# Optimization experiments

Hardware: AMD Instinct MI355X
Metric: run time of the kernel (lower is better)

Reference implementation:

```python
import jax, jax.numpy as jnp
import numpy as np

N_NODES = 100000
N_EDGES = 1600000
N_GRAPHS = 1024
DIM_IN = 128
DIM_SELF = 16
BN_EPS = 1e-5


def _bn(x, gamma, beta):
    # training-mode BatchNorm1d over dim 0 (biased variance, as torch uses for normalization)
    m = jnp.mean(x, axis=0)
    v = jnp.mean((x - m) ** 2, axis=0)
    return gamma * (x - m) * jax.lax.rsqrt(v + BN_EPS) + beta


def _mlp(x, W1, b1, g, b, W2, b2):
    h = x @ W1 + b1
    h = jax.nn.relu(_bn(h, g, b))
    return h @ W2 + b2


def _gin(h, src, dst, W1, b1, g, b, W2, b2):
    # GINConv with eps=0: (1+eps)*h + sum over in-neighbors, then MLP
    agg = jax.ops.segment_sum(h[src], dst, num_segments=N_NODES)
    return _mlp(h + agg, W1, b1, g, b, W2, b2)


def setup_inputs() -> dict:
    key = jax.random.key(0)
    ks = jax.random.split(key, 16)

    def lin(k, fan_in, fan_out):
        bound = 1.0 / np.sqrt(fan_in)
        k1, k2 = jax.random.split(k)
        W = jax.random.uniform(k1, (fan_in, fan_out), jnp.float32, -bound, bound)
        b = jax.random.uniform(k2, (fan_out,), jnp.float32, -bound, bound)
        return W, b

    inp = {}
    inp['feat'] = jax.random.normal(ks[0], (N_NODES, DIM_IN), jnp.float32)
    inp['self_feat'] = jax.random.normal(ks[1], (N_GRAPHS, DIM_SELF), jnp.float32)
    inp['edge_src'] = jax.random.randint(ks[2], (N_EDGES,), 0, N_NODES, jnp.int32)
    inp['edge_dst'] = jax.random.randint(ks[3], (N_EDGES,), 0, N_NODES, jnp.int32)
    inp['node2graph'] = jnp.sort(jax.random.randint(ks[4], (N_NODES,), 0, N_GRAPHS, jnp.int32))

    inp['g1_W1'], inp['g1_b1'] = lin(ks[5], DIM_IN, 100)
    inp['g1_gamma'] = jnp.ones((100,), jnp.float32)
    inp['g1_beta'] = jnp.zeros((100,), jnp.float32)
    inp['g1_W2'], inp['g1_b2'] = lin(ks[6], 100, 100)

    inp['g2_W1'], inp['g2_b1'] = lin(ks[7], 100, 20)
    inp['g2_gamma'] = jnp.ones((20,), jnp.float32)
    inp['g2_beta'] = jnp.zeros((20,), jnp.float32)
    inp['g2_W2'], inp['g2_b2'] = lin(ks[8], 20, 20)

    inp['fc1_W'], inp['fc1_b'] = lin(ks[9], 20 * DIM_SELF, 32)
    inp['bn1_gamma'] = jnp.ones((32,), jnp.float32)
    inp['bn1_beta'] = jnp.zeros((32,), jnp.float32)
    inp['fc2_W'], inp['fc2_b'] = lin(ks[10], 32, 8)
    inp['bn2_gamma'] = jnp.ones((8,), jnp.float32)
    inp['bn2_beta'] = jnp.zeros((8,), jnp.float32)
    inp['fc3_W'], inp['fc3_b'] = lin(ks[11], 8, 1)
    return inp


def reference(feat, self_feat,
              g1_W1, g1_b1, g1_gamma, g1_beta, g1_W2, g1_b2,
              g2_W1, g2_b1, g2_gamma, g2_beta, g2_W2, g2_b2,
              fc1_W, fc1_b, bn1_gamma, bn1_beta,
              fc2_W, fc2_b, bn2_gamma, bn2_beta,
              fc3_W, fc3_b,
              edge_src, edge_dst, node2graph):
    h = _gin(feat, edge_src, edge_dst, g1_W1, g1_b1, g1_gamma, g1_beta, g1_W2, g1_b2)
    h = jax.nn.relu(h)
    h = _gin(h, edge_src, edge_dst, g2_W1, g2_b1, g2_gamma, g2_beta, g2_W2, g2_b2)
    h = jax.nn.relu(h)  # [N, 20]

    # dgl.mean_nodes: per-graph mean of node features
    sums = jax.ops.segment_sum(h, node2graph, num_segments=N_GRAPHS)  # [B, 20]
    cnts = jax.ops.segment_sum(jnp.ones((N_NODES,), h.dtype), node2graph, num_segments=N_GRAPHS)
    hg = sums / jnp.maximum(cnts, 1.0)[:, None]

    # kronecker fusion: bmm([B,20,1],[B,1,dim_self]) -> flatten
    kron = jnp.einsum('bi,bj->bij', hg, self_feat).reshape(N_GRAPHS, -1)  # [B, 20*dim_self]

    out = jax.nn.relu(_bn(kron @ fc1_W + fc1_b, bn1_gamma, bn1_beta))
    # dropout(0.3) is identity in eval mode
    out = jax.nn.relu(_bn(out @ fc2_W + fc2_b, bn2_gamma, bn2_beta))
    out = out @ fc3_W + fc3_b  # [B, dim_out]
    return out
```

## Files before the change

### kernel.cpp

```cpp
#include <hip/hip_runtime.h>

#define NN 100000
#define NE 1600000
#define NG 1024
#define DIN 128
#define D1 100
#define D2 20
#define DSELF 16
#define BN_EPS 1e-5f

#define NB 391
#define NBLK 782
#define EPB 2048
#define RAWCAP 5120
#define NAGG2 4000
#define NREP 64
#define APITCH 136
#define G1BLK 1563

typedef unsigned int uint;
typedef unsigned short ushort;
typedef __attribute__((ext_vector_type(8))) short bfv8;
typedef __attribute__((ext_vector_type(4))) float fv4;

__device__ inline float bflo(uint x) { return __uint_as_float(x << 16); }
__device__ inline float bfhi(uint x) { return __uint_as_float(x & 0xffff0000u); }
__device__ inline float bfval(ushort h) { return __uint_as_float(((uint)h) << 16); }
__device__ inline uint packbf2(float a, float b) {
    uint ua = __float_as_uint(a), ub = __float_as_uint(b);
    ua += 0x7fffu + ((ua >> 16) & 1u);
    ub += 0x7fffu + ((ub >> 16) & 1u);
    return (ua >> 16) | (ub & 0xffff0000u);
}
__device__ inline ushort bfr(float x) {
    uint u = __float_as_uint(x);
    u += 0x7fffu + ((u >> 16) & 1u);
    return (ushort)(u >> 16);
}

__global__ __launch_bounds__(256) void k_gemm1A1(const float* __restrict__ feat,
                                                 const float* __restrict__ W1,
                                                 ushort* __restrict__ z1bf,
                                                 float* __restrict__ pb1r,
                                                 const int* __restrict__ edst,
                                                 int* __restrict__ pbcount,
                                                 const float* __restrict__ W2,
                                                 const float* __restrict__ W1p,
                                                 ushort* __restrict__ W2fh,
                                                 ushort* __restrict__ W2fl,
                                                 ushort* __restrict__ W1pfh,
                                                 ushort* __restrict__ W1pfl) {
    __shared__ __align__(16) char smem[64 * APITCH * 2 + 112 * APITCH * 2];
    int t = threadIdx.x;
    int blk = blockIdx.x;
    if (blk >= G1BLK) {
        int hb = blk - G1BLK;
        int* h = (int*)smem;
        if (hb < 9) {
#pragma unroll
            for (int i2 = 0; i2 < 8; i2++) {
                int idx = hb * 2048 + i2 * 256 + t;
                int l = (idx >> 3) & 63, j = idx & 7;
                int kq = (l >> 4) * 8 + j;
                int n16 = l & 15;
                if (idx < 14336) {
                    int tile = idx >> 9; int nt = tile >> 2, kk = tile & 3;
                    int k = kk * 32 + kq, n = nt * 16 + n16;
                    float v = (k < 100 && n < 100) ? W2[k * 100 + n] : 0.f;
                    ushort hh = bfr(v);
                    W2fh[idx] = hh; W2fl[idx] = bfr(v - bfval(hh));
                } else {
                    int idx2 = idx - 14336;
                    int tile = idx2 >> 9; int nt = tile >> 2, kk = tile & 3;
                    int k = kk * 32 + kq, n = nt * 16 + n16;
                    float v = (k < 100 && n < 20) ? W1p[k * 20 + n] : 0.f;
                    ushort hh = bfr(v);
                    W1pfh[idx2] = hh; W1pfl[idx2] = bfr(v - bfval(hh));
                }
            }
        }
        for (int i = t; i < NB; i += 256) h[i] = 0;
        __syncthreads();
        int e0 = hb * EPB + t;
#pragma unroll
        for (int i = 0; i < 8; i++) {
            int e = e0 + i * 256;
            if (e < NE) atomicAdd(&h[edst[e] >> 8], 1);
        }
        __syncthreads();
        for (int i = t; i < NB; i += 256) pbcount[i * NBLK + hb] = h[i];
        return;
    }
    ushort* Al = (ushort*)smem;
    ushort* Bt = (ushort*)(smem + 64 * APITCH * 2);
    if (blk == 0) {
        for (int i = t; i < NREP * 200; i += 256) pb1r[i] = 0.f;
    }
    int row0 = blk * 64;
#pragma unroll
    for (int i = 0; i < 8; i++) {
        int p = i * 256 + t;
        int r = p >> 5, cq = p & 31;
        int row = row0 + r; if (row >= NN) row = NN - 1;
        float4 v = *(const float4*)(feat + (size_t)row * DIN + cq * 4);
        ushort* dst = Al + r * APITCH + 4 * cq;
        dst[0] = bfr(v.x); dst[1] = bfr(v.y); dst[2] = bfr(v.z); dst[3] = bfr(v.w);
    }
    for (int p = t; p < 12800; p += 256) {
        int k = p / 100, n = p % 100;
        Bt[n * APITCH + k] = bfr(W1[p]);
    }
    __syncthreads();
    int w = __builtin_amdgcn_readfirstlane(t >> 6);
    int l = t & 63;
    int m16 = l & 15, quad = l >> 4;
    fv4 acc[7];
#pragma unroll
    for (int nt = 0; nt < 7; nt++) acc[nt] = (fv4){0.f, 0.f, 0.f, 0.f};
    const ushort* arow = Al + (w * 16 + m16) * APITCH;
#pragma unroll
    for (int kk = 0; kk < 4; kk++) {
        int kb = kk * 32 + quad * 8;
        bfv8 a = *(const bfv8*)(arow + kb);
#pragma unroll
        for (int nt = 0; nt < 7; nt++) {
            bfv8 b = *(const bfv8*)(Bt + (nt * 16 + m16) * APITCH + kb);
            acc[nt] = __builtin_amdgcn_mfma_f32_16x16x32_bf16(a, b, acc[nt], 0, 0, 0);
        }
    }
    __syncthreads();
    float* Ep = (float*)smem;
#pragma unroll
    for (int nt = 0; nt < 7; nt++) {
        int n = nt * 16 + m16;
        if (n < 100) {
#pragma unroll
            for (int rix = 0; rix < 4; rix++)
                Ep[(w * 16 + quad * 4 + rix) * 101 + n] = acc[nt][rix];
        }
    }
    __syncthreads();
#pragma unroll
    for (int i = 0; i < 13; i++) {
        int p = i * 256 + t;
        if (p < 3200) {
            int rr = p / 50, cc = 2 * (p % 50);
            int row = row0 + rr;
            if (row < NN) {
                float v0 = Ep[rr * 101 + cc], v1 = Ep[rr * 101 + cc + 1];
                *(uint*)(z1bf + (size_t)row * 128 + cc) = packbf2(v0, v1);
            }
        }
    }
}

__global__ __launch_bounds__(1024) void k_csrS1(int* __restrict__ pbcount,
                                                int* __restrict__ btot) {
    __shared__ int s[1024];
    int t = threadIdx.x, b = blockIdx.x;
    int v = (t < NBLK) ? pbcount[b * NBLK + t] : 0;
    s[t] = v;
    __syncthreads();
    for (int off = 1; off < 1024; off <<= 1) {
        int x = (t >= off) ? s[t - off] : 0;
        __syncthreads();
        s[t] += x;
        __syncthreads();
    }
    if (t < NBLK) pbcount[b * NBLK + t] = s[t] - v;
    if (t == 1023) btot[b] = s[t];
}

__global__ __launch_bounds__(256) void k_csrA2(const int* __restrict__ src,
                                               const int* __restrict__ dst,
                                               const int* __restrict__ pbexcl,
                                               const int* __restrict__ btot,
                                               int* __restrict__ ebase_g,
                                               uint* __restrict__ gbuf) {
    __shared__ int gb[NB];
    __shared__ int lo[NB];
    __shared__ int cnt[NB];
    __shared__ int sa[512], sb[512];
    __shared__ uint stage[EPB];
    __shared__ ushort bkts[EPB];
    int t = threadIdx.x, blk = blockIdx.x;
    int o0 = (t < NB) ? btot[t] : 0;
    int o1 = (t + 256 < NB) ? btot[t + 256] : 0;
    sa[t] = o0; sa[t + 256] = o1;
    if (t < NB) cnt[t] = 0;
    if (t + 256 < NB) cnt[t + 256] = 0;
    __syncthreads();
    int* sp = sa; int* dp = sb;
    for (int off = 1; off < 512; off <<= 1) {
        dp[t] = sp[t] + ((t >= off) ? sp[t - off] : 0);
        int i2 = t + 256;
        dp[i2] = sp[i2] + ((i2 >= off) ? sp[i2 - off] : 0);
        __syncthreads();
        int* tmp = sp; sp = dp; dp = tmp;
    }
    if (t < NB)       gb[t]       = (sp[t] - o0) + pbexcl[t * NBLK + blk];
    if (t + 256 < NB) gb[t + 256] = (sp[t + 256] - o1) + pbexcl[(t + 256) * NBLK + blk];
    if (blk == 0) {
        if (t < NB)       ebase_g[t]       = sp[t] - o0;
        if (t + 256 < NB) ebase_g[t + 256] = sp[t + 256] - o1;
        if (t == 0)       ebase_g[NB]      = sp[NB - 1];
    }
    __syncthreads();
    int e0 = blk * EPB + t;
    uint pv[8]; int bk[8];
#pragma unroll
    for (int i = 0; i < 8; i++) {
        int e = e0 + i * 256;
        if (e < NE) {
            int d = dst[e];
            bk[i] = d >> 8;
            pv[i] = (uint)src[e] | ((uint)(d & 255) << 17);
            atomicAdd(&cnt[bk[i]], 1);
        } else bk[i] = -1;
    }
    __syncthreads();
    sa[t] = (t < NB) ? cnt[t] : 0;
    sa[t + 256] = (t + 256 < NB) ? cnt[t + 256] : 0;
    __syncthreads();
    sp = sa; dp = sb;
    for (int off = 1; off < 512; off <<= 1) {
        dp[t] = sp[t] + ((t >= off) ? sp[t - off] : 0);
        int i2 = t + 256;
        dp[i2] = sp[i2] + ((i2 >= off) ? sp[i2 - off] : 0);
        __syncthreads();
        int* tmp = sp; sp = dp; dp = tmp;
    }
    if (t < NB)       lo[t]       = sp[t] - cnt[t];
    if (t + 256 < NB) lo[t + 256] = sp[t + 256] - cnt[t + 256];
    __syncthreads();
    if (t < NB) cnt[t] = 0;
    if (t + 256 < NB) cnt[t + 256] = 0;
    __syncthreads();
#pragma unroll
    for (int i = 0; i < 8; i++) {
        if (bk[i] >= 0) {
            int lpos = lo[bk[i]] + atomicAdd(&cnt[bk[i]], 1);
            stage[lpos] = pv[i];
            bkts[lpos] = (ushort)bk[i];
        }
    }
    __syncthreads();
    int cntb = (blk * EPB + EPB <= NE) ? EPB : (NE - blk * EPB);
    for (int i = t; i < cntb; i += 256) {
        int b = bkts[i];
        gbuf[gb[b] + (i - lo[b])] = stage[i];
    }
}

__global__ __launch_bounds__(256) void k_csrB(const uint* __restrict__ gbuf,
                                              const int* __restrict__ ebase,
                                              int* __restrict__ deg,
                                              int* __restrict__ offs,
                                              int* __restrict__ srcS) {
    __shared__ uint raw[RAWCAP];
    __shared__ int srt[RAWCAP];
    __shared__ int pref[256], cur[256];
    int t = threadIdx.x, b = blockIdx.x;
    int e0 = ebase[b], e1 = ebase[b + 1];
    int cnt = e1 - e0; if (cnt > RAWCAP) cnt = RAWCAP;
    cur[t] = 0;
    for (int i = t; i < cnt; i += 256) raw[i] = gbuf[e0 + i];
    __syncthreads();
    for (int i = t; i < cnt; i += 256) atomicAdd(&cur[raw[i] >> 17], 1);
    __syncthreads();
    int v = cur[t];
    pref[t] = v;
    __syncthreads();
    for (int off = 1; off < 256; off <<= 1) {
        int x = (t >= off) ? pref[t - off] : 0;
        __syncthreads();
        pref[t] += x;
        __syncthreads();
    }
    int excl = pref[t] - v;
    int node = b * 256 + t;
    if (node < NN) { deg[node] = v; offs[node] = e0 + excl; }
    cur[t] = excl;
    __syncthreads();
    for (int i = t; i < cnt; i += 256) {
        uint p = raw[i];
        int lpos = atomicAdd(&cur[p >> 17], 1);
        srt[lpos] = (int)(p & 0x1FFFFu);
    }
    __syncthreads();
    for (int i = t; i < cnt; i += 256) srcS[e0 + i] = srt[i];
}

__global__ __launch_bounds__(256) void k_agg1(const ushort* __restrict__ z1bf,
                                              const int* __restrict__ offs,
                                              const int* __restrict__ deg,
                                              const int* __restrict__ srcS,
                                              ushort* __restrict__ u1b,
                                              float* __restrict__ pb1r) {
    __shared__ float part[4][200];
    int t = threadIdx.x;
    int wv = __builtin_amdgcn_readfirstlane(t >> 6);
    int l = t & 63;
    bool act = l < 50;
    const ushort* zc = z1bf + 2 * l;
    float S0 = 0.f, S1 = 0.f, Q0 = 0.f, Q1 = 0.f;
    int n0 = blockIdx.x * 16 + wv * 4;
#pragma unroll 1
    for (int k = 0; k < 4; k++) {
        int n = n0 + k;
        int d = deg[n], base = offs[n];
        float a0 = 0.f, a1 = 0.f, b0 = 0.f, b1 = 0.f;
        float c0 = 0.f, c1 = 0.f, e0 = 0.f, e1 = 0.f;
        int i = 0;
        for (; i + 8 <= d; i += 8) {
            int s0 = srcS[base + i],     s1 = srcS[base + i + 1];
            int s2 = srcS[base + i + 2], s3 = srcS[base + i + 3];
            int s4 = srcS[base + i + 4], s5 = srcS[base + i + 5];
            int s6 = srcS[base + i + 6], s7 = srcS[base + i + 7];
            if (act) {
                uint x0 = *(const uint*)(zc + (size_t)s0 * 128);
                uint x1 = *(const uint*)(zc + (size_t)s1 * 128);
                uint x2 = *(const uint*)(zc + (size_t)s2 * 128);
                uint x3 = *(const uint*)(zc + (size_t)s3 * 128);
                uint x4 = *(const uint*)(zc + (size_t)s4 * 128);
                uint x5 = *(const uint*)(zc + (size_t)s5 * 128);
                uint x6 = *(const uint*)(zc + (size_t)s6 * 128);
                uint x7 = *(const uint*)(zc + (size_t)s7 * 128);
                a0 += bflo(x0); a1 += bfhi(x0);
                b0 += bflo(x1); b1 += bfhi(x1);
                c0 += bflo(x2); c1 += bfhi(x2);
                e0 += bflo(x3); e1 += bfhi(x3);
                a0 += bflo(x4); a1 += bfhi(x4);
                b0 += bflo(x5); b1 += bfhi(x5);
                c0 += bflo(x6); c1 += bfhi(x6);
                e0 += bflo(x7); e1 += bfhi(x7);
            }
        }
        for (; i + 2 <= d; i += 2) {
            int s0 = srcS[base + i], s1 = srcS[base + i + 1];
            if (act) {
                uint x0 = *(const uint*)(zc + (size_t)s0 * 128);
                uint x1 = *(const uint*)(zc + (size_t)s1 * 128);
                a0 += bflo(x0); a1 += bfhi(x0);
                b0 += bflo(x1); b1 += bfhi(x1);
            }
        }
        if (i < d) {
            int s0 = srcS[base + i];
            if (act) {
                uint x0 = *(const uint*)(zc + (size_t)s0 * 128);
                a0 += bflo(x0); a1 += bfhi(x0);
            }
        }
        if (act) {
            uint xs = *(const uint*)(zc + (size_t)n * 128);
            float r0 = (a0 + b0) + (c0 + e0) + bflo(xs);
            float r1 = (a1 + b1) + (c1 + e1) + bfhi(xs);
            *(uint*)(u1b + (size_t)n * 100 + 2 * l) = packbf2(r0, r1);
            S0 += r0; S1 += r1;
            Q0 = fmaf(r0, r0, Q0); Q1 = fmaf(r1, r1, Q1);
        }
    }
    if (act) {
        part[wv][2 * l] = S0;        part[wv][2 * l + 1] = S1;
        part[wv][100 + 2 * l] = Q0;  part[wv][100 + 2 * l + 1] = Q1;
    }
    __syncthreads();
    if (t < 200) {
        float s = part[0][t] + part[1][t] + part[2][t] + part[3][t];
        atomicAdd(&pb1r[(blockIdx.x & (NREP - 1)) * 200 + t], s);
    }
}

__global__ __launch_bounds__(256) void k_m2(const ushort* __restrict__ u1b,
                                            const float* __restrict__ pb1r,
                                            const float* __restrict__ gamma,
                                            const float* __restrict__ beta,
                                            const ushort* __restrict__ W2fh,
                                            const ushort* __restrict__ W2fl,
                                            const float* __restrict__ b2,
                                            const ushort* __restrict__ W1pfh,
                                            const ushort* __restrict__ W1pfl,
                                            ushort* __restrict__ z2bf,
                                            float* __restrict__ pb2r,
                                            float* __restrict__ hgsum) {
    __shared__ __align__(16) ushort Ah[64 * APITCH];
    __shared__ __align__(16) ushort Alo[64 * APITCH];
    __shared__ float red200[200];
    __shared__ float scW[100], shW[100];
    int t = threadIdx.x;
    if (blockIdx.x == 0) {
        for (int i = t; i < NREP * 40; i += 256) pb2r[i] = 0.f;
        for (int i = t; i < NG * D2; i += 256) hgsum[i] = 0.f;
    }
    if (t < 200) {
        float s = 0.f;
#pragma unroll 8
        for (int r = 0; r < NREP; r++) s += pb1r[r * 200 + t];
        red200[t] = s;
    }
    for (int p = t; p < 896; p += 256) {
        int r = p / 14, c = 100 + 2 * (p % 14);
        *(uint*)(Ah + r * APITCH + c) = 0u;
        *(uint*)(Alo + r * APITCH + c) = 0u;
    }
    __syncthreads();
    if (t < 100) {
        float S = red200[t], Q = red200[100 + t];
        float mean = S * (1.f / NN);
        float var = Q * (1.f / NN) - mean * mean;
        float inv = rsqrtf(var + BN_EPS);
        float s = gamma[t] * inv;
        scW[t] = s;
        shW[t] = beta[t] - mean * s;
    }
    __syncthreads();
    int row0 = blockIdx.x * 64;
#pragma unroll
    for (int i = 0; i < 13; i++) {
        int p = i * 256 + t;
        if (p < 3200) {
            int r = p / 50, c = 2 * (p % 50);
            int row = row0 + r; if (row >= NN) row = NN - 1;
            uint x = *(const uint*)(u1b + (size_t)row * 100 + c);
            float y0 = fmaxf(bflo(x) * scW[c] + shW[c], 0.f);
            float y1 = fmaxf(bfhi(x) * scW[c + 1] + shW[c + 1], 0.f);
            ushort h0 = bfr(y0), h1 = bfr(y1);
            ushort l0 = bfr(y0 - bfval(h0)), l1 = bfr(y1 - bfval(h1));
            *(uint*)(Ah + r * APITCH + c) = (uint)h0 | ((uint)h1 << 16);
            *(uint*)(Alo + r * APITCH + c) = (uint)l0 | ((uint)l1 << 16);
        }
    }
    __syncthreads();
    int w = __builtin_amdgcn_readfirstlane(t >> 6);
    int l = t & 63;
    int m16 = l & 15, quad = l >> 4;
    fv4 acc[7];
#pragma unroll
    for (int nt = 0; nt < 7; nt++) acc[nt] = (fv4){0.f, 0.f, 0.f, 0.f};
    {
        const ushort* arH = Ah + (w * 16 + m16) * APITCH;
        const ushort* arL = Alo + (w * 16 + m16) * APITCH;
#pragma unroll
        for (int kk = 0; kk < 4; kk++) {
            int kb = kk * 32 + quad * 8;
            bfv8 ah = *(const bfv8*)(arH + kb);
            bfv8 al = *(const bfv8*)(arL + kb);
#pragma unroll
            for (int nt = 0; nt < 7; nt++) {
                int fo = ((nt * 4 + kk) << 9) + l * 8;
                bfv8 bh = *(const bfv8*)(W2fh + fo);
                bfv8 bl = *(const bfv8*)(W2fl + fo);
                acc[nt] = __builtin_amdgcn_mfma_f32_16x16x32_bf16(ah, bh, acc[nt], 0, 0, 0);
                acc[nt] = __builtin_amdgcn_mfma_f32_16x16x32_bf16(ah, bl, acc[nt], 0, 0, 0);
                acc[nt] = __builtin_amdgcn_mfma_f32_16x16x32_bf16(al, bh, acc[nt], 0, 0, 0);
            }
        }
    }
    __syncthreads();
#pragma unroll
    for (int nt = 0; nt < 7; nt++) {
        int n = nt * 16 + m16;
        float bb = (n < 100) ? b2[n] : 0.f;
#pragma unroll
        for (int rix = 0; rix < 4; rix++) {
            int r = w * 16 + quad * 4 + rix;
            float hv = (n < 100) ? fmaxf(acc[nt][rix] + bb, 0.f) : 0.f;
            ushort hh = bfr(hv);
            Ah[r * APITCH + n] = hh;
            Alo[r * APITCH + n] = bfr(hv - bfval(hh));
        }
    }
    __syncthreads();
    fv4 acc2[2];
    acc2[0] = (fv4){0.f, 0.f, 0.f, 0.f};
    acc2[1] = (fv4){0.f, 0.f, 0.f, 0.f};
    {
        const ushort* arH = Ah + (w * 16 + m16) * APITCH;
        const ushort* arL = Alo + (w * 16 + m16) * APITCH;
#pragma unroll
        for (int kk = 0; kk < 4; kk++) {
            int kb = kk * 32 + quad * 8;
            bfv8 ah = *(const bfv8*)(arH + kb);
            bfv8 al = *(const bfv8*)(arL + kb);
#pragma unroll
            for (int nt = 0; nt < 2; nt++) {
                int fo = ((nt * 4 + kk) << 9) + l * 8;
                bfv8 bh = *(const bfv8*)(W1pfh + fo);
                bfv8 bl = *(const bfv8*)(W1pfl + fo);
                acc2[nt] = __builtin_amdgcn_mfma_f32_16x16x32_bf16(ah, bh, acc2[nt], 0, 0, 0);
                acc2[nt] = __builtin_amdgcn_mfma_f32_16x16x32_bf16(ah, bl, acc2[nt], 0, 0, 0);
                acc2[nt] = __builtin_amdgcn_mfma_f32_16x16x32_bf16(al, bh, acc2[nt], 0, 0, 0);
            }
        }
    }
#pragma unroll
    for (int nt = 0; nt < 2; nt++) {
        int c = nt * 16 + m16;
        if (c < 20) {
#pragma unroll
            for (int rix = 0; rix < 4; rix++) {
                int row = row0 + w * 16 + quad * 4 + rix;
                if (row < NN) z2bf[(size_t)row * 32 + c] = bfr(acc2[nt][rix]);
            }
        }
    }
}

__global__ __launch_bounds__(256) void k_agg2(const ushort* __restrict__ z2bf,
                                              const int* __restrict__ offs,
                                              const int* __restrict__ deg,
                                              const int* __restrict__ srcS,
                                              float* __restrict__ u2,
                                              float* __restrict__ pb2r) {
    __shared__ float ls[500], lq[500];
    int t = threadIdx.x;
    int n = blockIdx.x * 25 + t / 10;
    int c2 = 2 * (t % 10);
    float r0 = 0.f, r1 = 0.f;
    if (t < 250 && n < NN) {
        int d = deg[n], base = offs[n];
        const ushort* zc = z2bf + c2;
        float a0 = 0.f, a1 = 0.f, b0 = 0.f, b1 = 0.f;
        float c0 = 0.f, c1 = 0.f, e0 = 0.f, e1 = 0.f;
        int i = 0;
        for (; i + 8 <= d; i += 8) {
            int s0 = srcS[base + i],     s1 = srcS[base + i + 1];
            int s2 = srcS[base + i + 2], s3 = srcS[base + i + 3];
            int s4 = srcS[base + i + 4], s5 = srcS[base + i + 5];
            int s6 = srcS[base + i + 6], s7 = srcS[base + i + 7];
            uint x0 = *(const uint*)(zc + (size_t)s0 * 32);
            uint x1 = *(const uint*)(zc + (size_t)s1 * 32);
            uint x2 = *(const uint*)(zc + (size_t)s2 * 32);
            uint x3 = *(const uint*)(zc + (size_t)s3 * 32);
            uint x4 = *(const uint*)(zc + (size_t)s4 * 32);
            uint x5 = *(const uint*)(zc + (size_t)s5 * 32);
            uint x6 = *(const uint*)(zc + (size_t)s6 * 32);
            uint x7 = *(const uint*)(zc + (size_t)s7 * 32);
            a0 += bflo(x0); a1 += bfhi(x0);
            b0 += bflo(x1); b1 += bfhi(x1);
            c0 += bflo(x2); c1 += bfhi(x2);
            e0 += bflo(x3); e1 += bfhi(x3);
            a0 += bflo(x4); a1 += bfhi(x4);
            b0 += bflo(x5); b1 += bfhi(x5);
            c0 += bflo(x6); c1 += bfhi(x6);
            e0 += bflo(x7); e1 += bfhi(x7);
        }
        for (; i + 2 <= d; i += 2) {
            uint x0 = *(const uint*)(zc + (size_t)srcS[base + i] * 32);
            uint x1 = *(const uint*)(zc + (size_t)srcS[base + i + 1] * 32);
            a0 += bflo(x0); a1 += bfhi(x0);
            b0 += bflo(x1); b1 += bfhi(x1);
        }
        if (i < d) {
            uint x0 = *(const uint*)(zc + (size_t)srcS[base + i] * 32);
            a0 += bflo(x0); a1 += bfhi(x0);
        }
        uint xs = *(const uint*)(zc + (size_t)n * 32);
        r0 = (a0 + b0) + (c0 + e0) + bflo(xs);
        r1 = (a1 + b1) + (c1 + e1) + bfhi(xs);
        *(float2*)(u2 + (size_t)n * D2 + c2) = make_float2(r0, r1);
    }
    if (t < 250) {
        int idx = (t / 10) * 20 + c2;
        ls[idx] = r0;     lq[idx] = r0 * r0;
        ls[idx + 1] = r1; lq[idx + 1] = r1 * r1;
    }
    __syncthreads();
    if (t < 20) {
        float S = 0.f, Q = 0.f;
#pragma unroll
        for (int j = 0; j < 25; j++) { S += ls[j * 20 + t]; Q += lq[j * 20 + t]; }
        int rep = (blockIdx.x & (NREP - 1)) * 40;
        atomicAdd(&pb2r[rep + t], S);
        atomicAdd(&pb2r[rep + 20 + t], Q);
    }
}

__global__ __launch_bounds__(256) void k_m3p(const float* __restrict__ u2,
                                             const float* __restrict__ pb2r,
                                             const float* __restrict__ gamma,
                                             const float* __restrict__ beta,
                                             const float* __restrict__ W2p,
                                             const float* __restrict__ b2p,
                                             const int* __restrict__ n2g,
                                             float* __restrict__ hgsum) {
    __shared__ float X[256][21];
    __shared__ int gl[256];
    __shared__ float red40[40], scB[20], shB[20];
    int t = threadIdx.x;
    if (t < 40) {
        float s = 0.f;
#pragma unroll 8
        for (int r = 0; r < NREP; r++) s += pb2r[r * 40 + t];
        red40[t] = s;
    }
    __syncthreads();
    if (t < 20) {
        float S = red40[t], Q = red40[20 + t];
        float mean = S * (1.f / NN);
        float var = Q * (1.f / NN) - mean * mean;
        float inv = rsqrtf(var + BN_EPS);
        float s = gamma[t] * inv;
        scB[t] = s;
        shB[t] = beta[t] - mean * s;
    }
    __syncthreads();
    int row = blockIdx.x * 256 + t;
    bool valid = row < NN;
    gl[t] = valid ? n2g[row] : -1;
    if (valid) {
        float ya[20];
        const float4* up = (const float4*)(u2 + (size_t)row * D2);
#pragma unroll
        for (int i = 0; i < 5; i++) {
            float4 v = up[i];
            ya[4 * i + 0] = fmaxf(v.x * scB[4 * i + 0] + shB[4 * i + 0], 0.f);
            ya[4 * i + 1] = fmaxf(v.y * scB[4 * i + 1] + shB[4 * i + 1], 0.f);
            ya[4 * i + 2] = fmaxf(v.z * scB[4 * i + 2] + shB[4 * i + 2], 0.f);
            ya[4 * i + 3] = fmaxf(v.w * scB[4 * i + 3] + shB[4 * i + 3], 0.f);
        }
#pragma unroll
        for (int j = 0; j < D2; j++) {
            float h = b2p[j];
#pragma unroll
            for (int k = 0; k < D2; k++) h = fmaf(ya[k], W2p[k * D2 + j], h);
            X[t][j] = fmaxf(h, 0.f);
        }
    } else {
#pragma unroll
        for (int j = 0; j < D2; j++) X[t][j] = 0.f;
    }
    __syncthreads();
    if (t < 160) {
        int seg = t / 20, j = t % 20;
        int i0 = seg * 32, i1 = i0 + 32;
        int gprev = -2;
        float acc = 0.f;
        for (int i = i0; i < i1; i++) {
            int gi = gl[i];
            if (gi != gprev) {
                if (gprev >= 0) atomicAdd(&hgsum[gprev * D2 + j], acc);
                gprev = gi; acc = 0.f;
            }
            acc += X[i][j];
        }
        if (gprev >= 0) atomicAdd(&hgsum[gprev * D2 + j], acc);
    }
}

__global__ void k_head1(const float* __restrict__ hgsum, const int* __restrict__ n2g,
                        const float* __restrict__ sf,
                        const float* __restrict__ fc1W, float* __restrict__ a1) {
    int b = blockIdx.x * 8 + threadIdx.x / 32;
    int c = threadIdx.x % 32;
    if (b >= NG) return;
    int lo = 0, hi2 = NN;
    while (lo < hi2) { int mid = (lo + hi2) >> 1; if (n2g[mid] < b) lo = mid + 1; else hi2 = mid; }
    int s0 = lo;
    hi2 = NN;
    while (lo < hi2) { int mid = (lo + hi2) >> 1; if (n2g[mid] < b + 1) lo = mid + 1; else hi2 = mid; }
    float rc = 1.f / fmaxf((float)(lo - s0), 1.f);
    const float* hgb = hgsum + b * D2;
    const float* sfb = sf + b * DSELF;
    float acc = 0.f;
    for (int i = 0; i < D2; i++) {
        float hv = hgb[i] * rc;
#pragma unroll
        for (int j = 0; j < DSELF; j++)
            acc += hv * sfb[j] * fc1W[(i * DSELF + j) * 32 + c];
    }
    a1[b * 32 + c] = acc;
}

__global__ __launch_bounds__(1024) void k_head2(
    const float* __restrict__ a1, const float* __restrict__ g1,
    const float* __restrict__ be1, const float* __restrict__ fc2W,
    const float* __restrict__ g2, const float* __restrict__ be2,
    const float* __restrict__ fc3W, const float* __restrict__ fc3b,
    float* __restrict__ out) {
    int t = threadIdx.x;
    int lane = t & 63, w = t >> 6;
    __shared__ float s1[16][32], s2[16][32];
    __shared__ float sc[32], sh[32], sc2[8], sh2[8];
    float x[32];
    const float4* ap = (const float4*)(a1 + t * 32);
#pragma unroll
    for (int i = 0; i < 8; i++) {
        float4 v = ap[i];
        x[4 * i] = v.x; x[4 * i + 1] = v.y; x[4 * i + 2] = v.z; x[4 * i + 3] = v.w;
    }
#pragma unroll
    for (int c = 0; c < 32; c++) {
        float v = x[c], q = v * v;
        for (int o = 32; o > 0; o >>= 1) {
            v += __shfl_down(v, o, 64);
            q += __shfl_down(q, o, 64);
        }
        if (lane == 0) { s1[w][c] = v; s2[w][c] = q; }
    }
    __syncthreads();
    if (t < 32) {
        float s = 0.f, q = 0.f;
        for (int ww = 0; ww < 16; ww++) { s += s1[ww][t]; q += s2[ww][t]; }
        float mean = s * (1.f / NG);
        float var = q * (1.f / NG) - mean * mean;
        float inv = rsqrtf(var + BN_EPS);
        float scl = g1[t] * inv;
        sc[t] = scl;
        sh[t] = be1[t] - mean * scl;
    }
    __syncthreads();
#pragma unroll
    for (int c = 0; c < 32; c++) x[c] = fmaxf(x[c] * sc[c] + sh[c], 0.f);
    float y[8];
#pragma unroll
    for (int p = 0; p < 8; p++) {
        float a = 0.f;
#pragma unroll
        for (int c = 0; c < 32; c++) a += x[c] * fc2W[c * 8 + p];
        y[p] = a;
    }
    __syncthreads();
#pragma unroll
    for (int p = 0; p < 8; p++) {
        float v = y[p], q = v * v;
        for (int o = 32; o > 0; o >>= 1) {
            v += __shfl_down(v, o, 64);
            q += __shfl_down(q, o, 64);
        }
        if (lane == 0) { s1[w][p] = v; s2[w][p] = q; }
    }
    __syncthreads();
    if (t < 8) {
        float s = 0.f, q = 0.f;
        for (int ww = 0; ww < 16; ww++) { s += s1[ww][t]; q += s2[ww][t]; }
        float mean = s * (1.f / NG);
        float var = q * (1.f / NG) - mean * mean;
        float inv = rsqrtf(var + BN_EPS);
        float scl = g2[t] * inv;
        sc2[t] = scl;
        sh2[t] = be2[t] - mean * scl;
    }
    __syncthreads();
    float o = fc3b[0];
#pragma unroll
    for (int p = 0; p < 8; p++) {
        float yy = fmaxf(y[p] * sc2[p] + sh2[p], 0.f);
        o += yy * fc3W[p];
    }
    out[t] = o;
}

extern "C" void kernel_launch(void* const* d_in, const int* in_sizes, int n_in,
                              void* d_out, int out_size, void* d_ws, size_t ws_size,
                              hipStream_t stream) {
    const float* feat    = (const float*)d_in[0];
    const float* sf      = (const float*)d_in[1];
    const int*   esrc    = (const int*)d_in[2];
    const int*   edst    = (const int*)d_in[3];
    const int*   n2g     = (const int*)d_in[4];
    const float* g1W1    = (const float*)d_in[5];
    const float* g1gam   = (const float*)d_in[7];
    const float* g1bet   = (const float*)d_in[8];
    const float* g1W2    = (const float*)d_in[9];
    const float* g1b2    = (const float*)d_in[10];
    const float* g2W1    = (const float*)d_in[11];
    const float* g2gam   = (const float*)d_in[13];
    const float* g2bet   = (const float*)d_in[14];
    const float* g2W2    = (const float*)d_in[15];
    const float* g2b2    = (const float*)d_in[16];
    const float* fc1W    = (const float*)d_in[17];
    const float* hbn1g   = (const float*)d_in[19];
    const float* hbn1b   = (const float*)d_in[20];
    const float* fc2W    = (const float*)d_in[21];
    const float* hbn2g   = (const float*)d_in[23];
    const float* hbn2b   = (const float*)d_in[24];
    const float* fc3W    = (const float*)d_in[25];
    const float* fc3b    = (const float*)d_in[26];
    float* out = (float*)d_out;

    char* w = (char*)d_ws;
    size_t off = 0;
    auto alloc = [&](size_t bytes) -> char* {
        char* p = w + off;
        off += (bytes + 15) & ~(size_t)15;
        return p;
    };
    char* regA = alloc((size_t)NN * 128 * 2);
    ushort* z1bf = (ushort*)regA;
    ushort* z2bf = (ushort*)regA;
    float*  u2   = (float*)(regA + 6400000);
    ushort* u1b  = (ushort*)alloc((size_t)NN * 100 * 2);
    int*   pbcnt = (int*)alloc((size_t)NB * NBLK * 4);
    int*   btot  = (int*)alloc(NB * 4);
    int*   ebase = (int*)alloc((NB + 1) * 4);
    uint*  gbuf  = (uint*)alloc((size_t)NE * 4);
    int*   deg   = (int*)alloc(NN * 4);
    int*   offs  = (int*)alloc(NN * 4);
    int*   srcS  = (int*)alloc((size_t)NE * 4);
    float* pb1r  = (float*)alloc((size_t)NREP * 200 * 4);
    float* pb2r  = (float*)alloc((size_t)NREP * 40 * 4);
    ushort* W2fh = (ushort*)alloc(14336 * 2);
    ushort* W2fl = (ushort*)alloc(14336 * 2);
    ushort* W1pfh = (ushort*)alloc(4096 * 2);
    ushort* W1pfl = (ushort*)alloc(4096 * 2);
    float* hgsum = (float*)alloc((size_t)NG * D2 * 4);
    float* a1    = (float*)alloc(NG * 32 * 4);
    (void)in_sizes; (void)n_in; (void)out_size; (void)ws_size;

    k_gemm1A1<<<G1BLK + NBLK, 256, 0, stream>>>(feat, g1W1, z1bf, pb1r, edst, pbcnt,
                                                g1W2, g2W1, W2fh, W2fl, W1pfh, W1pfl);
    k_csrS1<<<NB, 1024, 0, stream>>>(pbcnt, btot);
    k_csrA2<<<NBLK, 256, 0, stream>>>(esrc, edst, pbcnt, btot, ebase, gbuf);
    k_csrB<<<NB, 256, 0, stream>>>(gbuf, ebase, deg, offs, srcS);

    k_agg1<<<NN / 16, 256, 0, stream>>>(z1bf, offs, deg, srcS, u1b, pb1r);

    k_m2<<<G1BLK, 256, 0, stream>>>(u1b, pb1r, g1gam, g1bet, W2fh, W2fl, g1b2,
                                    W1pfh, W1pfl, z2bf, pb2r, hgsum);

    k_agg2<<<NAGG2, 256, 0, stream>>>(z2bf, offs, deg, srcS, u2, pb2r);
    k_m3p<<<(NN + 255) / 256, 256, 0, stream>>>(u2, pb2r, g2gam, g2bet, g2W2, g2b2, n2g, hgsum);

    k_head1<<<NG / 8, 256, 0, stream>>>(hgsum, n2g, sf, fc1W, a1);
    k_head2<<<1, 1024, 0, stream>>>(a1, hbn1g, hbn1b, fc2W, hbn2g, hbn2b, fc3W, fc3b, out);
}
```

Measured before the change: 372.9 us.

## Pre-swizzle W1 into MFMA fragment layout; split edges across half-waves in agg1

A new prep kernel converts the first-layer W1 to bf16 in MFMA fragment order once, along with the other weight swizzles and the pb1r zeroing. Previously every gemm1 block rebuilt a transposed bf16 copy of W1 in shared memory. The GEMM now reads B fragments straight from global memory, which cuts per-block LDS staging and shrinks shared memory use. In agg1, each wave is split into two halves of 25 lanes that handle alternating edges with 8-byte loads, and the halves are combined by shuffle. This raises bytes per load and puts more gathers in flight, at the cost of an extra launch and shuffle work.

```diff
diff --git a/kernel.cpp b/kernel.cpp
--- a/kernel.cpp
+++ b/kernel.cpp
@@ -38,47 +38,52 @@
     return (ushort)(u >> 16);
 }
 
+__global__ __launch_bounds__(256) void k_prep(const float* __restrict__ W1,
+                                              const float* __restrict__ W2,
+                                              const float* __restrict__ W1p,
+                                              ushort* __restrict__ W1f,
+                                              ushort* __restrict__ W2fh,
+                                              ushort* __restrict__ W2fl,
+                                              ushort* __restrict__ W1pfh,
+                                              ushort* __restrict__ W1pfl,
+                                              float* __restrict__ pb1r) {
+    int idx = blockIdx.x * 256 + threadIdx.x;
+    if (idx < NREP * 200) pb1r[idx] = 0.f;
+    if (idx < 14336) {
+        int tile = idx >> 9, nt = tile >> 2, kk = tile & 3;
+        int l = (idx >> 3) & 63, j = idx & 7;
+        int k = kk * 32 + (l >> 4) * 8 + j, n = nt * 16 + (l & 15);
+        W1f[idx] = bfr((n < 100) ? W1[k * 100 + n] : 0.f);
+    } else if (idx < 28672) {
+        int x = idx - 14336;
+        int tile = x >> 9, nt = tile >> 2, kk = tile & 3;
+        int l = (x >> 3) & 63, j = x & 7;
+        int k = kk * 32 + (l >> 4) * 8 + j, n = nt * 16 + (l & 15);
+        float v = (k < 100 && n < 100) ? W2[k * 100 + n] : 0.f;
+        ushort hh = bfr(v);
+        W2fh[x] = hh; W2fl[x] = bfr(v - bfval(hh));
+    } else if (idx < 32768) {
+        int x = idx - 28672;
+        int tile = x >> 9, nt = tile >> 2, kk = tile & 3;
+        int l = (x >> 3) & 63, j = x & 7;
+        int k = kk * 32 + (l >> 4) * 8 + j, n = nt * 16 + (l & 15);
+        float v = (k < 100 && n < 20) ? W1p[k * 20 + n] : 0.f;
+        ushort hh = bfr(v);
+        W1pfh[x] = hh; W1pfl[x] = bfr(v - bfval(hh));
+    }
+}
+
 __global__ __launch_bounds__(256) void k_gemm1A1(const float* __restrict__ feat,
-                                                 const float* __restrict__ W1,
+                                                 const ushort* __restrict__ W1f,
                                                  ushort* __restrict__ z1bf,
-                                                 float* __restrict__ pb1r,
                                                  const int* __restrict__ edst,
-                                                 int* __restrict__ pbcount,
-                                                 const float* __restrict__ W2,
-                                                 const float* __restrict__ W1p,
-                                                 ushort* __restrict__ W2fh,
-                                                 ushort* __restrict__ W2fl,
-                                                 ushort* __restrict__ W1pfh,
-                                                 ushort* __restrict__ W1pfl) {
-    __shared__ __align__(16) char smem[64 * APITCH * 2 + 112 * APITCH * 2];
+                                                 int* __restrict__ pbcount) {
+    __shared__ __align__(16) char smem[64 * 101 * 4];
     int t = threadIdx.x;
     int blk = blockIdx.x;
     if (blk >= G1BLK) {
         int hb = blk - G1BLK;
         int* h = (int*)smem;
-        if (hb < 9) {
-#pragma unroll
-            for (int i2 = 0; i2 < 8; i2++) {
-                int idx = hb * 2048 + i2 * 256 + t;
-                int l = (idx >> 3) & 63, j = idx & 7;
-                int kq = (l >> 4) * 8 + j;
-                int n16 = l & 15;
-                if (idx < 14336) {
-                    int tile = idx >> 9; int nt = tile >> 2, kk = tile & 3;
-                    int k = kk * 32 + kq, n = nt * 16 + n16;
-                    float v = (k < 100 && n < 100) ? W2[k * 100 + n] : 0.f;
-                    ushort hh = bfr(v);
-                    W2fh[idx] = hh; W2fl[idx] = bfr(v - bfval(hh));
-                } else {
-                    int idx2 = idx - 14336;
-                    int tile = idx2 >> 9; int nt = tile >> 2, kk = tile & 3;
-                    int k = kk * 32 + kq, n = nt * 16 + n16;
-                    float v = (k < 100 && n < 20) ? W1p[k * 20 + n] : 0.f;
-                    ushort hh = bfr(v);
-                    W1pfh[idx2] = hh; W1pfl[idx2] = bfr(v - bfval(hh));
-                }
-            }
-        }
         for (int i = t; i < NB; i += 256) h[i] = 0;
         __syncthreads();
         int e0 = hb * EPB + t;
@@ -92,10 +97,6 @@
         return;
     }
     ushort* Al = (ushort*)smem;
-    ushort* Bt = (ushort*)(smem + 64 * APITCH * 2);
-    if (blk == 0) {
-        for (int i = t; i < NREP * 200; i += 256) pb1r[i] = 0.f;
-    }
     int row0 = blk * 64;
 #pragma unroll
     for (int i = 0; i < 8; i++) {
@@ -106,10 +107,6 @@
         ushort* dst = Al + r * APITCH + 4 * cq;
         dst[0] = bfr(v.x); dst[1] = bfr(v.y); dst[2] = bfr(v.z); dst[3] = bfr(v.w);
     }
-    for (int p = t; p < 12800; p += 256) {
-        int k = p / 100, n = p % 100;
-        Bt[n * APITCH + k] = bfr(W1[p]);
-    }
     __syncthreads();
     int w = __builtin_amdgcn_readfirstlane(t >> 6);
     int l = t & 63;
@@ -124,7 +121,7 @@
         bfv8 a = *(const bfv8*)(arow + kb);
 #pragma unroll
         for (int nt = 0; nt < 7; nt++) {
-            bfv8 b = *(const bfv8*)(Bt + (nt * 16 + m16) * APITCH + kb);
+            bfv8 b = *(const bfv8*)(W1f + ((nt * 4 + kk) << 9) + l * 8);
             acc[nt] = __builtin_amdgcn_mfma_f32_16x16x32_bf16(a, b, acc[nt], 0, 0, 0);
         }
     }
@@ -301,69 +298,74 @@
     int t = threadIdx.x;
     int wv = __builtin_amdgcn_readfirstlane(t >> 6);
     int l = t & 63;
+    int p = (l >= 25) ? 1 : 0;
+    int c = l - 25 * p;
     bool act = l < 50;
-    const ushort* zc = z1bf + 2 * l;
-    float S0 = 0.f, S1 = 0.f, Q0 = 0.f, Q1 = 0.f;
+    const ushort* zc = z1bf + 4 * c;
+    float S0 = 0.f, S1 = 0.f, S2 = 0.f, S3 = 0.f;
+    float Q0 = 0.f, Q1 = 0.f, Q2 = 0.f, Q3 = 0.f;
     int n0 = blockIdx.x * 16 + wv * 4;
 #pragma unroll 1
     for (int k = 0; k < 4; k++) {
         int n = n0 + k;
         int d = deg[n], base = offs[n];
-        float a0 = 0.f, a1 = 0.f, b0 = 0.f, b1 = 0.f;
-        float c0 = 0.f, c1 = 0.f, e0 = 0.f, e1 = 0.f;
+        float a0 = 0.f, a1 = 0.f, a2 = 0.f, a3 = 0.f;
+        float b0 = 0.f, b1 = 0.f, b2 = 0.f, b3 = 0.f;
         int i = 0;
         for (; i + 8 <= d; i += 8) {
-            int s0 = srcS[base + i],     s1 = srcS[base + i + 1];
-            int s2 = srcS[base + i + 2], s3 = srcS[base + i + 3];
-            int s4 = srcS[base + i + 4], s5 = srcS[base + i + 5];
-            int s6 = srcS[base + i + 6], s7 = srcS[base + i + 7];
+            int sa = srcS[base + i + p];
+            int sb = srcS[base + i + 2 + p];
+            int sc = srcS[base + i + 4 + p];
+            int sd = srcS[base + i + 6 + p];
             if (act) {
-                uint x0 = *(const uint*)(zc + (size_t)s0 * 128);
-                uint x1 = *(const uint*)(zc + (size_t)s1 * 128);
-                uint x2 = *(const uint*)(zc + (size_t)s2 * 128);
-                uint x3 = *(const uint*)(zc + (size_t)s3 * 128);
-                uint x4 = *(const uint*)(zc + (size_t)s4 * 128);
-                uint x5 = *(const uint*)(zc + (size_t)s5 * 128);
-                uint x6 = *(const uint*)(zc + (size_t)s6 * 128);
-                uint x7 = *(const uint*)(zc + (size_t)s7 * 128);
-                a0 += bflo(x0); a1 += bfhi(x0);
-                b0 += bflo(x1); b1 += bfhi(x1);
-                c0 += bflo(x2); c1 += bfhi(x2);
-                e0 += bflo(x3); e1 += bfhi(x3);
-                a0 += bflo(x4); a1 += bfhi(x4);
-                b0 += bflo(x5); b1 += bfhi(x5);
-                c0 += bflo(x6); c1 += bfhi(x6);
-                e0 += bflo(x7); e1 += bfhi(x7);
+                uint2 x0 = *(const uint2*)(zc + (size_t)sa * 128);
+                uint2 x1 = *(const uint2*)(zc + (size_t)sb * 128);
+                uint2 x2 = *(const uint2*)(zc + (size_t)sc * 128);
+                uint2 x3 = *(const uint2*)(zc + (size_t)sd * 128);
+                a0 += bflo(x0.x); a1 += bfhi(x0.x); a2 += bflo(x0.y); a3 += bfhi(x0.y);
+                b0 += bflo(x1.x); b1 += bfhi(x1.x); b2 += bflo(x1.y); b3 += bfhi(x1.y);
+                a0 += bflo(x2.x); a1 += bfhi(x2.x); a2 += bflo(x2.y); a3 += bfhi(x2.y);
+                b0 += bflo(x3.x); b1 += bfhi(x3.x); b2 += bflo(x3.y); b3 += bfhi(x3.y);
             }
         }
         for (; i + 2 <= d; i += 2) {
-            int s0 = srcS[base + i], s1 = srcS[base + i + 1];
+            int sa = srcS[base + i + p];
             if (act) {
-                uint x0 = *(const uint*)(zc + (size_t)s0 * 128);
-                uint x1 = *(const uint*)(zc + (size_t)s1 * 128);
-                a0 += bflo(x0); a1 += bfhi(x0);
-                b0 += bflo(x1); b1 += bfhi(x1);
+                uint2 x0 = *(const uint2*)(zc + (size_t)sa * 128);
+                a0 += bflo(x0.x); a1 += bfhi(x0.x); a2 += bflo(x0.y); a3 += bfhi(x0.y);
             }
         }
         if (i < d) {
-            int s0 = srcS[base + i];
-            if (act) {
-                uint x0 = *(const uint*)(zc + (size_t)s0 * 128);
-                a0 += bflo(x0); a1 += bfhi(x0);
+            int sa = srcS[base + i];
+            if (act && p == 0) {
+                uint2 x0 = *(const uint2*)(zc + (size_t)sa * 128);
+                b0 += bflo(x0.x); b1 += bfhi(x0.x); b2 += bflo(x0.y); b3 += bfhi(x0.y);
             }
         }
-        if (act) {
-            uint xs = *(const uint*)(zc + (size_t)n * 128);
-            float r0 = (a0 + b0) + (c0 + e0) + bflo(xs);
-            float r1 = (a1 + b1) + (c1 + e1) + bfhi(xs);
-            *(uint*)(u1b + (size_t)n * 100 + 2 * l) = packbf2(r0, r1);
-            S0 += r0; S1 += r1;
+        if (act && p == 1) {
+            uint2 xs = *(const uint2*)(zc + (size_t)n * 128);
+            b0 += bflo(xs.x); b1 += bfhi(xs.x); b2 += bflo(xs.y); b3 += bfhi(xs.y);
+        }
+        float r0 = a0 + b0, r1 = a1 + b1, r2 = a2 + b2, r3 = a3 + b3;
+        int partner = (p == 0) ? (l + 25) : (l - 25);
+        r0 += __shfl(r0, partner, 64);
+        r1 += __shfl(r1, partner, 64);
+        r2 += __shfl(r2, partner, 64);
+        r3 += __shfl(r3, partner, 64);
+        if (act && p == 0) {
+            uint2 o;
+            o.x = packbf2(r0, r1); o.y = packbf2(r2, r3);
+            *(uint2*)(u1b + (size_t)n * 100 + 4 * c) = o;
+            S0 += r0; S1 += r1; S2 += r2; S3 += r3;
             Q0 = fmaf(r0, r0, Q0); Q1 = fmaf(r1, r1, Q1);
-        }
-    }
-    if (act) {
-        part[wv][2 * l] = S0;        part[wv][2 * l + 1] = S1;
-        part[wv][100 + 2 * l] = Q0;  part[wv][100 + 2 * l + 1] = Q1;
+            Q2 = fmaf(r2, r2, Q2); Q3 = fmaf(r3, r3, Q3);
+        }
+    }
+    if (act && p == 0) {
+        part[wv][4 * c + 0] = S0; part[wv][4 * c + 1] = S1;
+        part[wv][4 * c + 2] = S2; part[wv][4 * c + 3] = S3;
+        part[wv][100 + 4 * c + 0] = Q0; part[wv][100 + 4 * c + 1] = Q1;
+        part[wv][100 + 4 * c + 2] = Q2; part[wv][100 + 4 * c + 3] = Q3;
     }
     __syncthreads();
     if (t < 200) {
@@ -801,6 +803,7 @@
     int*   srcS  = (int*)alloc((size_t)NE * 4);
     float* pb1r  = (float*)alloc((size_t)NREP * 200 * 4);
     float* pb2r  = (float*)alloc((size_t)NREP * 40 * 4);
+    ushort* W1f  = (ushort*)alloc(14336 * 2);
     ushort* W2fh = (ushort*)alloc(14336 * 2);
     ushort* W2fl = (ushort*)alloc(14336 * 2);
     ushort* W1pfh = (ushort*)alloc(4096 * 2);
@@ -809,8 +812,9 @@
     float* a1    = (float*)alloc(NG * 32 * 4);
     (void)in_sizes; (void)n_in; (void)out_size; (void)ws_size;
 
-    k_gemm1A1<<<G1BLK + NBLK, 256, 0, stream>>>(feat, g1W1, z1bf, pb1r, edst, pbcnt,
-                                                g1W2, g2W1, W2fh, W2fl, W1pfh, W1pfl);
+    k_prep<<<128, 256, 0, stream>>>(g1W1, g1W2, g2W1, W1f, W2fh, W2fl, W1pfh, W1pfl, pb1r);
+
+    k_gemm1A1<<<G1BLK + NBLK, 256, 0, stream>>>(feat, W1f, z1bf, edst, pbcnt);
     k_csrS1<<<NB, 1024, 0, stream>>>(pbcnt, btot);
     k_csrA2<<<NBLK, 256, 0, stream>>>(esrc, edst, pbcnt, btot, ebase, gbuf);
     k_csrB<<<NB, 256, 0, stream>>>(gbuf, ebase, deg, offs, srcS);
```

Result: no change. 370.0 us (-0.8%).
